# Kernel tuning notes

Hardware: AMD Instinct MI355X
Metric: run time of the kernel (lower is better)

## Reference

```python
import jax, jax.numpy as jnp
import numpy as np

NUM_CLASSES = 21
BATCH = 128
ANCHORS = 8732


def setup_inputs() -> dict:
    key = jax.random.key(0)
    k1, k2, k3, k4 = jax.random.split(key, 4)
    loc_preds = jax.random.normal(k1, (BATCH, ANCHORS, 4), dtype=jnp.float32)
    loc_targets = jax.random.normal(k2, (BATCH, ANCHORS, 4), dtype=jnp.float32)
    cls_preds = jax.random.normal(k3, (BATCH, ANCHORS, NUM_CLASSES), dtype=jnp.float32)
    cls_targets = jax.random.randint(k4, (BATCH, ANCHORS), 0, NUM_CLASSES, dtype=jnp.int64)
    return {
        "loc_preds": loc_preds,
        "loc_targets": loc_targets,
        "cls_preds": cls_preds,
        "cls_targets": cls_targets,
    }


def _ssd_loss(loc_preds, loc_targets, cls_preds, cls_targets):
    pos = cls_targets > 0                                   # [B, A] bool
    num_pos = pos.sum().astype(loc_preds.dtype)

    # masked smooth-L1 (beta = 1.0), sum reduction over positive anchors
    diff = jnp.abs(loc_preds - loc_targets)                 # [B, A, 4]
    sl1 = jnp.where(diff < 1.0, 0.5 * diff * diff, diff - 0.5)
    loc_loss = jnp.sum(sl1 * pos[..., None].astype(sl1.dtype))

    # per-anchor cross entropy
    logp = jax.nn.log_softmax(cls_preds, axis=-1)           # [B, A, C]
    tgt = jnp.clip(cls_targets, 0, NUM_CLASSES - 1)
    ce = -jnp.take_along_axis(logp, tgt[..., None], axis=-1)[..., 0]  # [B, A]
    ce = jnp.where(cls_targets < 0, 0.0, ce)

    # hard negative mining via double argsort (rank of each anchor's loss)
    mined = ce * (pos.astype(ce.dtype) - 1.0)               # 0 at pos, -loss at neg
    idx = jnp.argsort(mined, axis=1)
    rank = jnp.argsort(idx, axis=1)
    num_pos_per = pos.sum(axis=1, keepdims=True)            # [B, 1]
    neg = rank < 3 * num_pos_per                            # [B, A]

    cls_loss = jnp.sum(jnp.where(pos | neg, ce, 0.0))
    return (loc_loss + cls_loss) / num_pos


def reference(loc_preds, loc_targets, cls_preds, cls_targets):
    return _ssd_loss(loc_preds, loc_targets, cls_preds, cls_targets)
```

## Files before the change

kernel.cpp:

```cpp
#include <hip/hip_runtime.h>
#include <stdint.h>

namespace {

constexpr int B  = 128;
constexpr int A  = 8732;
constexpr int NC = 21;
constexpr int TM = 128;
constexpr int THREADS = 256;
constexpr int ABLK = (A + TM - 1) / TM;
constexpr int NBLK = ABLK * B;

__device__ __forceinline__ float waveReduceSum(float v) {
#pragma unroll
    for (int off = 32; off; off >>= 1) v += __shfl_xor(v, off, 64);
    return v;
}
__device__ __forceinline__ int waveReduceSumI(int v) {
#pragma unroll
    for (int off = 32; off; off >>= 1) v += __shfl_xor(v, off, 64);
    return v;
}

__global__ __launch_bounds__(TM) void main_kernel(
    const float* __restrict__ locp,
    const float* __restrict__ loct,
    const float* __restrict__ clsp,
    const int*   __restrict__ tgt,
    float* __restrict__ locPart,
    float* __restrict__ clsPart,
    int*   __restrict__ posPart)
{
    const int b  = blockIdx.y;
    const int a0 = blockIdx.x * TM;
    const int rem = (A - a0 < TM) ? (A - a0) : TM;
    const int lane = threadIdx.x & 63;

    __shared__ __align__(16) float scls[TM * NC];
    {
        const float4* __restrict__ src = (const float4*)(clsp + ((long)b * A + a0) * NC);
        const int nf4 = rem * NC / 4;
        for (int idx = threadIdx.x; idx < nf4; idx += TM) {
            __builtin_amdgcn_global_load_lds(
                (const __attribute__((address_space(1))) void*)(src + idx),
                (__attribute__((address_space(3))) void*)(scls + (idx - lane) * 4),
                16, 0, 0);
        }
    }

    int t = 0;
    float4 lp = make_float4(0.f, 0.f, 0.f, 0.f);
    float4 lt = make_float4(0.f, 0.f, 0.f, 0.f);
    const long i = (long)b * A + (a0 + threadIdx.x);
    if (threadIdx.x < rem) {
        t  = tgt[i];
        lp = *(const float4*)(locp + i * 4);
        lt = *(const float4*)(loct + i * 4);
    }

    __syncthreads();

    float ce = 0.f, locv = 0.f;
    int posc = 0;

    if (threadIdx.x < rem) {
        const float* __restrict__ x = scls + threadIdx.x * NC;
        float xs[NC];
#pragma unroll
        for (int c = 0; c < NC; ++c) xs[c] = x[c];
        float m = xs[0];
#pragma unroll
        for (int c = 1; c < NC; ++c) m = fmaxf(m, xs[c]);
        float s = 0.f;
#pragma unroll
        for (int c = 0; c < NC; ++c) s += __expf(xs[c] - m);
        const int tc = t < 0 ? 0 : (t > NC - 1 ? NC - 1 : t);
        ce = (t < 0) ? 0.f : (m + __logf(s) - xs[tc]);

        if (t > 0) {
            posc = 1;
            float d;
            d = fabsf(lp.x - lt.x); locv += (d < 1.f) ? 0.5f * d * d : d - 0.5f;
            d = fabsf(lp.y - lt.y); locv += (d < 1.f) ? 0.5f * d * d : d - 0.5f;
            d = fabsf(lp.z - lt.z); locv += (d < 1.f) ? 0.5f * d * d : d - 0.5f;
            d = fabsf(lp.w - lt.w); locv += (d < 1.f) ? 0.5f * d * d : d - 0.5f;
        }
    }

    __shared__ float sLoc[2], sCls[2];
    __shared__ int sPos[2];
    const int wid = threadIdx.x >> 6;
    float wl = waveReduceSum(locv);
    float wc = waveReduceSum(ce);
    int   wp = waveReduceSumI(posc);
    if (lane == 0) { sLoc[wid] = wl; sCls[wid] = wc; sPos[wid] = wp; }
    __syncthreads();
    if (threadIdx.x == 0) {
        const int blk = b * gridDim.x + blockIdx.x;
        locPart[blk] = sLoc[0] + sLoc[1];
        clsPart[blk] = sCls[0] + sCls[1];
        posPart[blk] = sPos[0] + sPos[1];
    }
}

__global__ __launch_bounds__(THREADS) void mining_kernel(
    const float* __restrict__ clsp,
    const int*   __restrict__ tgt,
    const int*   __restrict__ posPart,
    float* __restrict__ corr)
{
    const int b = blockIdx.x;
    const int wid = threadIdx.x >> 6, lane = threadIdx.x & 63;

    int cnt = (threadIdx.x < ABLK) ? posPart[b * ABLK + threadIdx.x] : 0;
    __shared__ int sCnt[4];
    int wcnt = waveReduceSumI(cnt);
    if (lane == 0) sCnt[wid] = wcnt;
    __syncthreads();
    const int K = 3 * (sCnt[0] + sCnt[1] + sCnt[2] + sCnt[3]);

    float corrv = 0.f;
    if (K < A) {
        __shared__ float mined[A];
        for (int i = threadIdx.x; i < A; i += THREADS) {
            const long idx = (long)b * A + i;
            const int t = tgt[idx];
            float ce = 0.f;
            if (t >= 0) {
                const float* __restrict__ x = clsp + idx * (long)NC;
                float m = x[0];
                for (int c = 1; c < NC; ++c) m = fmaxf(m, x[c]);
                float s = 0.f;
                for (int c = 0; c < NC; ++c) s += __expf(x[c] - m);
                const int tc = t > NC - 1 ? NC - 1 : t;
                ce = m + __logf(s) - x[tc];
            }
            mined[i] = (t > 0) ? 0.f : -ce;
        }
        __syncthreads();

        float c0 = 0.f;
        for (int i = threadIdx.x; i < A; i += THREADS) {
            const int t = tgt[(long)b * A + i];
            if (t > 0) continue;
            const float mi = mined[i];
            int rank = 0;
            for (int j = 0; j < A; ++j) {
                const float mj = mined[j];
                rank += (mj < mi || (mj == mi && j < i)) ? 1 : 0;
            }
            if (rank >= K) c0 += mi;
        }
        __shared__ float sC[4];
        float wcorr = waveReduceSum(c0);
        if (lane == 0) sC[wid] = wcorr;
        __syncthreads();
        corrv = sC[0] + sC[1] + sC[2] + sC[3];
    }
    if (threadIdx.x == 0) corr[b] = corrv;
}

__global__ __launch_bounds__(THREADS) void finalize_kernel(
    const float* __restrict__ locPart,
    const float* __restrict__ clsPart,
    const int*   __restrict__ posPart,
    const float* __restrict__ corr,
    float* __restrict__ out)
{
    float L = 0.f, C = 0.f;
    int P = 0;
    for (int i = threadIdx.x; i < NBLK; i += THREADS) {
        L += locPart[i];
        C += clsPart[i];
        P += posPart[i];
    }
    if (threadIdx.x < B) C += corr[threadIdx.x];

    __shared__ float sL[4], sC[4];
    __shared__ int sP[4];
    const int wid = threadIdx.x >> 6, lane = threadIdx.x & 63;
    float wl = waveReduceSum(L);
    float wc = waveReduceSum(C);
    int   wp = waveReduceSumI(P);
    if (lane == 0) { sL[wid] = wl; sC[wid] = wc; sP[wid] = wp; }
    __syncthreads();
    if (threadIdx.x == 0) {
        const float loc = sL[0] + sL[1] + sL[2] + sL[3];
        const float cls = sC[0] + sC[1] + sC[2] + sC[3];
        const int   np  = sP[0] + sP[1] + sP[2] + sP[3];
        out[0] = (loc + cls) / (float)np;
    }
}

}

extern "C" void kernel_launch(void* const* d_in, const int* in_sizes, int n_in,
                              void* d_out, int out_size, void* d_ws, size_t ws_size,
                              hipStream_t stream) {
    const float* locp = (const float*)d_in[0];
    const float* loct = (const float*)d_in[1];
    const float* clsp = (const float*)d_in[2];
    const int*   tgt  = (const int*)d_in[3];

    float* locPart = (float*)d_ws;
    float* clsPart = locPart + NBLK;
    int*   posPart = (int*)(clsPart + NBLK);
    float* corr    = (float*)(posPart + NBLK);
    float* out     = (float*)d_out;

    hipLaunchKernelGGL(main_kernel, dim3(ABLK, B), dim3(TM), 0, stream,
                       locp, loct, clsp, tgt, locPart, clsPart, posPart);
    hipLaunchKernelGGL(mining_kernel, dim3(B), dim3(THREADS), 0, stream,
                       clsp, tgt, posPart, corr);
    hipLaunchKernelGGL(finalize_kernel, dim3(1), dim3(THREADS), 0, stream,
                       locPart, clsPart, posPart, corr, out);
}
```

Measured before the change: 185.2 us.

## Make main kernel persistent with register-prefetched double buffering of class tiles

Replaces the one-tile-per-block main kernel with a grid of 16 blocks per batch row that loop over tiles. Each iteration loads the next tile's logits, targets and box data into registers while the current tile's softmax and loss are computed from LDS. This is meant to hide global load latency and cut the number of blocks and partial sums. The cost is more registers, two barriers per tile, lower parallelism, and no longer using direct global-to-LDS loads.

```diff
diff --git a/kernel.cpp b/kernel.cpp
--- a/kernel.cpp
+++ b/kernel.cpp
@@ -3,13 +3,15 @@
 
 namespace {
 
-constexpr int B  = 128;
-constexpr int A  = 8732;
-constexpr int NC = 21;
-constexpr int TM = 128;
+constexpr int B    = 128;
+constexpr int A    = 8732;
+constexpr int NC   = 21;
+constexpr int TILE = 128;
+constexpr int T    = 128;
+constexpr int TPR  = (A + TILE - 1) / TILE;
+constexpr int CH   = 16;
+constexpr int NBLK = B * CH;
 constexpr int THREADS = 256;
-constexpr int ABLK = (A + TM - 1) / TM;
-constexpr int NBLK = ABLK * B;
 
 __device__ __forceinline__ float waveReduceSum(float v) {
 #pragma unroll
@@ -22,7 +24,7 @@
     return v;
 }
 
-__global__ __launch_bounds__(TM) void main_kernel(
+__global__ __launch_bounds__(T) void main_kernel(
     const float* __restrict__ locp,
     const float* __restrict__ loct,
     const float* __restrict__ clsp,
@@ -31,72 +33,100 @@
     float* __restrict__ clsPart,
     int*   __restrict__ posPart)
 {
-    const int b  = blockIdx.y;
-    const int a0 = blockIdx.x * TM;
-    const int rem = (A - a0 < TM) ? (A - a0) : TM;
-    const int lane = threadIdx.x & 63;
-
-    __shared__ __align__(16) float scls[TM * NC];
-    {
-        const float4* __restrict__ src = (const float4*)(clsp + ((long)b * A + a0) * NC);
-        const int nf4 = rem * NC / 4;
-        for (int idx = threadIdx.x; idx < nf4; idx += TM) {
-            __builtin_amdgcn_global_load_lds(
-                (const __attribute__((address_space(1))) void*)(src + idx),
-                (__attribute__((address_space(3))) void*)(scls + (idx - lane) * 4),
-                16, 0, 0);
+    const int b   = blockIdx.y;
+    const int c   = blockIdx.x;
+    const int tid = threadIdx.x;
+    const long rowBase = (long)b * A;
+
+    __shared__ __align__(16) float scls[TILE * NC];
+    float4* const scls4 = (float4*)scls;
+
+    float accLoc = 0.f, accCe = 0.f;
+    int accPos = 0;
+
+    float4 r0, r1, r2, r3, r4, r5, lpN, ltN;
+    int tN = 0, nN = 0, nf4N = 0;
+
+    auto issue = [&](int tile) {
+        const int a0 = tile * TILE;
+        nN   = (A - a0 < TILE) ? (A - a0) : TILE;
+        nf4N = nN * NC / 4;
+        const float4* __restrict__ src = (const float4*)(clsp + (rowBase + a0) * NC);
+        r0 = src[tid];
+        if (tid + 1 * T < nf4N) r1 = src[tid + 1 * T];
+        if (tid + 2 * T < nf4N) r2 = src[tid + 2 * T];
+        if (tid + 3 * T < nf4N) r3 = src[tid + 3 * T];
+        if (tid + 4 * T < nf4N) r4 = src[tid + 4 * T];
+        if (tid + 5 * T < nf4N) r5 = src[tid + 5 * T];
+        if (tid < nN) {
+            const long i = rowBase + a0 + tid;
+            tN  = tgt[i];
+            lpN = *(const float4*)(locp + i * 4);
+            ltN = *(const float4*)(loct + i * 4);
+        } else tN = 0;
+    };
+    auto writeLds = [&](int nf4) {
+        scls4[tid] = r0;
+        if (tid + 1 * T < nf4) scls4[tid + 1 * T] = r1;
+        if (tid + 2 * T < nf4) scls4[tid + 2 * T] = r2;
+        if (tid + 3 * T < nf4) scls4[tid + 3 * T] = r3;
+        if (tid + 4 * T < nf4) scls4[tid + 4 * T] = r4;
+        if (tid + 5 * T < nf4) scls4[tid + 5 * T] = r5;
+    };
+
+    int tile = c;
+    issue(tile);
+    writeLds(nf4N);
+    __syncthreads();
+    float4 lp = lpN, lt = ltN;
+    int tt = tN, n = nN;
+
+    for (;;) {
+        const int nxt = tile + CH;
+        const bool hasNext = nxt < TPR;
+        if (hasNext) issue(nxt);
+
+        if (tid < n) {
+            const float* __restrict__ x = scls + tid * NC;
+            float xs[NC];
+#pragma unroll
+            for (int cc = 0; cc < NC; ++cc) xs[cc] = x[cc];
+            float m = xs[0];
+#pragma unroll
+            for (int cc = 1; cc < NC; ++cc) m = fmaxf(m, xs[cc]);
+            float s = 0.f;
+#pragma unroll
+            for (int cc = 0; cc < NC; ++cc) s += __expf(xs[cc] - m);
+            const int tc = tt < 0 ? 0 : (tt > NC - 1 ? NC - 1 : tt);
+            accCe += (tt < 0) ? 0.f : (m + __logf(s) - xs[tc]);
+            if (tt > 0) {
+                ++accPos;
+                float d;
+                d = fabsf(lp.x - lt.x); accLoc += (d < 1.f) ? 0.5f * d * d : d - 0.5f;
+                d = fabsf(lp.y - lt.y); accLoc += (d < 1.f) ? 0.5f * d * d : d - 0.5f;
+                d = fabsf(lp.z - lt.z); accLoc += (d < 1.f) ? 0.5f * d * d : d - 0.5f;
+                d = fabsf(lp.w - lt.w); accLoc += (d < 1.f) ? 0.5f * d * d : d - 0.5f;
+            }
         }
-    }
-
-    int t = 0;
-    float4 lp = make_float4(0.f, 0.f, 0.f, 0.f);
-    float4 lt = make_float4(0.f, 0.f, 0.f, 0.f);
-    const long i = (long)b * A + (a0 + threadIdx.x);
-    if (threadIdx.x < rem) {
-        t  = tgt[i];
-        lp = *(const float4*)(locp + i * 4);
-        lt = *(const float4*)(loct + i * 4);
-    }
-
-    __syncthreads();
-
-    float ce = 0.f, locv = 0.f;
-    int posc = 0;
-
-    if (threadIdx.x < rem) {
-        const float* __restrict__ x = scls + threadIdx.x * NC;
-        float xs[NC];
-#pragma unroll
-        for (int c = 0; c < NC; ++c) xs[c] = x[c];
-        float m = xs[0];
-#pragma unroll
-        for (int c = 1; c < NC; ++c) m = fmaxf(m, xs[c]);
-        float s = 0.f;
-#pragma unroll
-        for (int c = 0; c < NC; ++c) s += __expf(xs[c] - m);
-        const int tc = t < 0 ? 0 : (t > NC - 1 ? NC - 1 : t);
-        ce = (t < 0) ? 0.f : (m + __logf(s) - xs[tc]);
-
-        if (t > 0) {
-            posc = 1;
-            float d;
-            d = fabsf(lp.x - lt.x); locv += (d < 1.f) ? 0.5f * d * d : d - 0.5f;
-            d = fabsf(lp.y - lt.y); locv += (d < 1.f) ? 0.5f * d * d : d - 0.5f;
-            d = fabsf(lp.z - lt.z); locv += (d < 1.f) ? 0.5f * d * d : d - 0.5f;
-            d = fabsf(lp.w - lt.w); locv += (d < 1.f) ? 0.5f * d * d : d - 0.5f;
-        }
+        if (!hasNext) break;
+
+        __syncthreads();
+        writeLds(nf4N);
+        __syncthreads();
+        lp = lpN; lt = ltN; tt = tN; n = nN;
+        tile = nxt;
     }
 
     __shared__ float sLoc[2], sCls[2];
     __shared__ int sPos[2];
-    const int wid = threadIdx.x >> 6;
-    float wl = waveReduceSum(locv);
-    float wc = waveReduceSum(ce);
-    int   wp = waveReduceSumI(posc);
+    const int wid = tid >> 6, lane = tid & 63;
+    float wl = waveReduceSum(accLoc);
+    float wc = waveReduceSum(accCe);
+    int   wp = waveReduceSumI(accPos);
     if (lane == 0) { sLoc[wid] = wl; sCls[wid] = wc; sPos[wid] = wp; }
     __syncthreads();
-    if (threadIdx.x == 0) {
-        const int blk = b * gridDim.x + blockIdx.x;
+    if (tid == 0) {
+        const int blk = b * CH + c;
         locPart[blk] = sLoc[0] + sLoc[1];
         clsPart[blk] = sCls[0] + sCls[1];
         posPart[blk] = sPos[0] + sPos[1];
@@ -112,7 +142,7 @@
     const int b = blockIdx.x;
     const int wid = threadIdx.x >> 6, lane = threadIdx.x & 63;
 
-    int cnt = (threadIdx.x < ABLK) ? posPart[b * ABLK + threadIdx.x] : 0;
+    int cnt = (threadIdx.x < CH) ? posPart[b * CH + threadIdx.x] : 0;
     __shared__ int sCnt[4];
     int wcnt = waveReduceSumI(cnt);
     if (lane == 0) sCnt[wid] = wcnt;
@@ -129,9 +159,9 @@
             if (t >= 0) {
                 const float* __restrict__ x = clsp + idx * (long)NC;
                 float m = x[0];
-                for (int c = 1; c < NC; ++c) m = fmaxf(m, x[c]);
+                for (int cc = 1; cc < NC; ++cc) m = fmaxf(m, x[cc]);
                 float s = 0.f;
-                for (int c = 0; c < NC; ++c) s += __expf(x[c] - m);
+                for (int cc = 0; cc < NC; ++cc) s += __expf(x[cc] - m);
                 const int tc = t > NC - 1 ? NC - 1 : t;
                 ce = m + __logf(s) - x[tc];
             }
@@ -208,7 +238,7 @@
     float* corr    = (float*)(posPart + NBLK);
     float* out     = (float*)d_out;
 
-    hipLaunchKernelGGL(main_kernel, dim3(ABLK, B), dim3(TM), 0, stream,
+    hipLaunchKernelGGL(main_kernel, dim3(CH, B), dim3(T), 0, stream,
                        locp, loct, clsp, tgt, locPart, clsPart, posPart);
     hipLaunchKernelGGL(mining_kernel, dim3(B), dim3(THREADS), 0, stream,
                        clsp, tgt, posPart, corr);
```

After: 183.6 us. Within noise of the previous version (-0.9%).
